# Optimization experiments

Measured on AMD Instinct MI355X. Metric: run time of the kernel, lower is better.

The kernel has to match this reference:

```python
import jax, jax.numpy as jnp
import numpy as np

DIM = 1024      # main_dim
HEADS = 16      # attn_num
HEAD = DIM // HEADS
S = 1024        # seq len per half
BH = 1          # batch per half (x_input batch = 2*BH)
PE = 16; FE = 16      # experts per group
PD = 512; FD = 512    # expert hidden dims
DS = 2048             # shared_expert_dim
K = 4                 # top_k routed experts
EPS = 1e-5
THETA = 10000.0
SCALE_P = 1.0; SCALE_F = 1.0


def rmsnorm(x, w, eps=EPS):
    return x * jax.lax.rsqrt(jnp.mean(x * x, -1, keepdims=True) + eps) * w


def rope(x, theta=THETA):
    # x: [b, h, s, a]; matches RotaryEmb: y1 = x1*cos + x2*sin, y2 = -x1*sin + x2*cos
    a = x.shape[-1]; s = x.shape[2]
    inv = (1.0 / theta) ** (jnp.arange(0, a, 2, dtype=jnp.float32) / a)
    fr = jnp.arange(s, dtype=jnp.float32)[:, None] * inv[None, :]   # [s, a//2]
    cos, sin = jnp.cos(fr), jnp.sin(fr)
    x1, x2 = jnp.split(x, 2, -1)
    return jnp.concatenate([x1 * cos + x2 * sin, -x1 * sin + x2 * cos], -1)


def moe(xt, block, idx, sc):
    # xt: [T, d]; block: [3, E, d, f] (gate/up/down SwiGLU); idx, sc: [T, K]
    g = jnp.einsum('td,edf->tef', xt, block[0])
    u = jnp.einsum('td,edf->tef', xt, block[1])
    h = jax.nn.silu(g) * u
    out_all = jnp.einsum('tef,edf->ted', h, block[2])        # per-expert outputs
    sel = jnp.take_along_axis(out_all, idx[:, :, None], 1)   # [T, K, d]
    return jnp.sum(sel * sc[:, :, None], 1)


def setup_inputs():
    key = jax.random.key(0)
    ks = jax.random.split(key, 16)
    w = 0.02  # param scale for numerical sanity
    d = {}
    d['x_input'] = jax.random.normal(ks[0], (2 * BH, S, DIM), jnp.float32)
    d['p_indices'] = jax.random.randint(ks[1], (BH * S, K), 0, PE)
    d['p_values'] = jax.random.normal(ks[2], (BH * S, K), jnp.float32)
    d['f_indices'] = jax.random.randint(ks[3], (BH * S, K), 0, FE)
    d['f_values'] = jax.random.normal(ks[4], (BH * S, K), jnp.float32)
    d['attn_norm_w'] = jnp.ones((DIM,), jnp.float32)
    d['ffn_norm_w'] = jnp.ones((DIM,), jnp.float32)
    d['W_attn'] = jax.random.normal(ks[5], (DIM, 3 * DIM), jnp.float32) * w
    d['W_attn_o'] = jax.random.normal(ks[6], (DIM, DIM), jnp.float32) * w
    d['ffn_up_w'] = jax.random.normal(ks[7], (DIM, 2 * DS), jnp.float32) * w
    d['ffn_down_w'] = jax.random.normal(ks[8], (DS, DIM), jnp.float32) * w
    d['p_ffn_experts'] = jax.random.normal(ks[9], (3, PE, DIM, PD), jnp.float32) * w
    d['f_ffn_experts'] = jax.random.normal(ks[10], (3, FE, DIM, FD), jnp.float32) * w
    d['p_token_keys'] = jax.random.normal(ks[11], (DIM, PE), jnp.float32) * w
    d['f_token_keys'] = jax.random.normal(ks[12], (DIM, FE), jnp.float32) * w
    d['p_router_bias'] = jnp.zeros((PE,), jnp.float32)
    d['f_router_bias'] = jnp.zeros((FE,), jnp.float32)
    return d


def reference(x_input, p_indices, p_values, f_indices, f_values,
              attn_norm_w, ffn_norm_w, W_attn, W_attn_o, ffn_up_w, ffn_down_w,
              p_ffn_experts, f_ffn_experts, p_token_keys, f_token_keys,
              p_router_bias, f_router_bias):
    B2, s, dim = x_input.shape
    b = B2 // 2
    # attention block
    x = rmsnorm(x_input, attn_norm_w)
    xq, xk, xv = jnp.split(x @ W_attn, 3, -1)
    heads = lambda t: t.reshape(B2, s, HEADS, HEAD).transpose(0, 2, 1, 3)
    xq, xk, xv = heads(xq), heads(xk), heads(xv)
    xq, xk = rope(xq), rope(xk)
    # dual interleave: '(c b) h s a -> b h (s c) a', c=2
    il = lambda t: t.reshape(2, b, HEADS, s, HEAD).transpose(1, 2, 3, 0, 4).reshape(b, HEADS, 2 * s, HEAD)
    q, k, v = il(xq), il(xk), il(xv)
    scores = jnp.einsum('bhqa,bhka->bhqk', q, k) / jnp.sqrt(jnp.float32(HEAD))
    causal = jnp.tril(jnp.ones((2 * s, 2 * s), bool))
    attn = jax.nn.softmax(jnp.where(causal, scores, -jnp.inf), -1)
    o = jnp.einsum('bhqk,bhka->bhqa', attn, v)
    # de-interleave: 'b h (s c) a -> (c b) s (h a)'
    o = o.reshape(b, HEADS, s, 2, HEAD).transpose(3, 0, 2, 1, 4).reshape(B2, s, dim)
    x_ffn_input = o @ W_attn_o + x_input
    x_ffn = rmsnorm(x_ffn_input, ffn_norm_w)
    p_x = x_ffn[:b].reshape(-1, dim)
    f_x = x_ffn[b:].reshape(-1, dim)
    # router: token keys + bias, sigmoid, normalize
    p_vals = p_values + jnp.take_along_axis(p_x @ p_token_keys, p_indices, -1) + p_router_bias[p_indices]
    f_vals = f_values + jnp.take_along_axis(f_x @ f_token_keys, f_indices, -1) + f_router_bias[f_indices]
    p_sc = jax.nn.sigmoid(p_vals)
    p_sc = p_sc / jnp.sum(p_sc, -1, keepdims=True) * SCALE_P
    f_sc = jax.nn.sigmoid(f_vals)
    f_sc = f_sc / jnp.sum(f_sc, -1, keepdims=True) * SCALE_F
    py = moe(p_x, p_ffn_experts, p_indices, p_sc).reshape(b, s, dim)
    fy = moe(f_x, f_ffn_experts, f_indices, f_sc).reshape(b, s, dim)
    y = jnp.concatenate([py, fy], 0) + x_ffn_input
    # shared expert (SwiGLU)
    x1, x2 = jnp.split(x_ffn @ ffn_up_w, 2, -1)
    y = y + (jax.nn.silu(x1) * x2) @ ffn_down_w
    return y
```

## Files before the change

### kernel.cpp

```cpp
#include <hip/hip_runtime.h>


#define S_LEN   1024
#define T_TOT   2048
#define DMODEL  1024
#define NHEADS  16
#define HDIM    64
#define NEXP    16
#define FDIM    512
#define DSH     2048
#define TOPK    4
#define NPAIR   8192

typedef __attribute__((ext_vector_type(4))) float          f32x4;
typedef __attribute__((ext_vector_type(8))) short          s16x8;
typedef __attribute__((ext_vector_type(4))) unsigned short u16x4;

__device__ __forceinline__ float sigm(float x) { return 1.0f / (1.0f + __expf(-x)); }

__device__ __forceinline__ unsigned short bf16r(float f) {
    union { float f; unsigned int u; } v; v.f = f;
    unsigned int r = v.u + 0x7fffu + ((v.u >> 16) & 1u);
    return (unsigned short)(r >> 16);
}

__device__ __forceinline__ u16x4 pack4(float a, float b, float c, float d) {
    u16x4 r;
    r.x = bf16r(a); r.y = bf16r(b); r.z = bf16r(c); r.w = bf16r(d);
    return r;
}

__device__ __forceinline__ int pair2tok(int p) {
    return ((p >> 12) << 10) + ((p & 4095) >> 2);
}

__global__ void rmsnorm_kernel(const float* __restrict__ x,
                               const float* __restrict__ w,
                               float* __restrict__ out) {
    int t = blockIdx.x, tid = threadIdx.x;
    float4 xv = *(const float4*)(x + (size_t)t * DMODEL + tid * 4);
    __shared__ float rb[256];
    rb[tid] = xv.x*xv.x + xv.y*xv.y + xv.z*xv.z + xv.w*xv.w;
    __syncthreads();
    for (int s = 128; s > 0; s >>= 1) { if (tid < s) rb[tid] += rb[tid+s]; __syncthreads(); }
    float scale = rsqrtf(rb[0] * (1.0f/1024.0f) + 1e-5f);
    float4 wv = *(const float4*)(w + tid * 4);
    float4 o;
    o.x = xv.x * scale * wv.x;
    o.y = xv.y * scale * wv.y;
    o.z = xv.z * scale * wv.z;
    o.w = xv.w * scale * wv.w;
    *(float4*)(out + (size_t)t*DMODEL + tid*4) = o;
}

__global__ void rope_kernel(float* __restrict__ qkv) {
    int t = blockIdx.x, tid = threadIdx.x;
    int s = t & 1023;
    float* row = qkv + (size_t)t * 3072;
    for (int pp = tid; pp < 512; pp += 256) {
        int h = pp >> 5, i = pp & 31;
        float fr = (float)s * exp2f(-0.41524101186092028f * (float)i);
        float sn, cs;
        sincosf(fr, &sn, &cs);
        int o1 = (h << 6) + i, o2 = o1 + 32;
        float x1 = row[o1], x2 = row[o2];
        row[o1] = x1 * cs + x2 * sn;
        row[o2] = x2 * cs - x1 * sn;
        x1 = row[1024 + o1]; x2 = row[1024 + o2];
        row[1024 + o1] = x1 * cs + x2 * sn;
        row[1024 + o2] = x2 * cs - x1 * sn;
    }
}

__global__ __launch_bounds__(256) void attn_mfma_kernel(
        const float* __restrict__ qkv, float* __restrict__ attn_out) {
    int qt = blockIdx.x, h = blockIdx.y;
    __shared__ alignas(16) unsigned short Qs[64][72];
    __shared__ alignas(16) unsigned short Ks[64][72];
    __shared__ alignas(16) unsigned short Vt[64][72];
    __shared__ alignas(16) unsigned short Ps[4][16][72];
    int tid = threadIdx.x;
    int w = tid >> 6, lane = tid & 63;
    int lr = lane & 15, lkg = lane >> 4, lk = lkg << 3;

    int rrj[4], ccj[4];
    #pragma unroll
    for (int j = 0; j < 4; ++j) {
        int idx = tid * 4 + j * 1024;
        rrj[j] = idx >> 6; ccj[j] = idx & 63;
    }

    #pragma unroll
    for (int j = 0; j < 4; ++j) {
        int p = qt * 64 + rrj[j];
        int t = ((p & 1) << 10) + (p >> 1);
        float4 v = *(const float4*)(qkv + (size_t)t * 3072 + (h << 6) + ccj[j]);
        *(u16x4*)&Qs[rrj[j]][ccj[j]] = pack4(v.x * 0.125f, v.y * 0.125f,
                                             v.z * 0.125f, v.w * 0.125f);
    }
    float4 pk[4], pv[4];
    #pragma unroll
    for (int j = 0; j < 4; ++j) {
        int p = rrj[j];
        int t = ((p & 1) << 10) + (p >> 1);
        const float* b = qkv + (size_t)t * 3072 + (h << 6) + ccj[j];
        pk[j] = *(const float4*)(b + 1024);
        pv[j] = *(const float4*)(b + 2048);
    }
    __syncthreads();
    s16x8 qa0 = *(const s16x8*)&Qs[(w << 4) + lr][lk];
    s16x8 qa1 = *(const s16x8*)&Qs[(w << 4) + lr][32 + lk];

    float m[4], l[4];
    f32x4 oacc[4];
    #pragma unroll
    for (int r = 0; r < 4; ++r) { m[r] = -1e30f; l[r] = 0.0f; }
    #pragma unroll
    for (int df = 0; df < 4; ++df) oacc[df] = (f32x4)0.0f;

    int qrow_base = qt * 64 + w * 16 + lkg * 4;

    for (int kb = 0; kb <= qt; ++kb) {
        __syncthreads();
        float4 ck[4], cv[4];
        #pragma unroll
        for (int j = 0; j < 4; ++j) { ck[j] = pk[j]; cv[j] = pv[j]; }
        if (kb + 1 <= qt) {
            #pragma unroll
            for (int j = 0; j < 4; ++j) {
                int p = (kb + 1) * 64 + rrj[j];
                int t = ((p & 1) << 10) + (p >> 1);
                const float* b = qkv + (size_t)t * 3072 + (h << 6) + ccj[j];
                pk[j] = *(const float4*)(b + 1024);
                pv[j] = *(const float4*)(b + 2048);
            }
        }
        #pragma unroll
        for (int j = 0; j < 4; ++j) {
            int rr = rrj[j], cc = ccj[j];
            *(u16x4*)&Ks[rr][cc] = pack4(ck[j].x, ck[j].y, ck[j].z, ck[j].w);
            Vt[cc + 0][rr] = bf16r(cv[j].x);
            Vt[cc + 1][rr] = bf16r(cv[j].y);
            Vt[cc + 2][rr] = bf16r(cv[j].z);
            Vt[cc + 3][rr] = bf16r(cv[j].w);
        }
        __syncthreads();

        f32x4 s[4];
        #pragma unroll
        for (int nf = 0; nf < 4; ++nf) {
            s16x8 b0 = *(const s16x8*)&Ks[nf * 16 + lr][lk];
            s16x8 b1 = *(const s16x8*)&Ks[nf * 16 + lr][32 + lk];
            f32x4 z = (f32x4)0.0f;
            z = __builtin_amdgcn_mfma_f32_16x16x32_bf16(qa0, b0, z, 0, 0, 0);
            z = __builtin_amdgcn_mfma_f32_16x16x32_bf16(qa1, b1, z, 0, 0, 0);
            s[nf] = z;
        }
        if (kb == qt) {
            #pragma unroll
            for (int nf = 0; nf < 4; ++nf) {
                int kcol = kb * 64 + nf * 16 + lr;
                #pragma unroll
                for (int r = 0; r < 4; ++r)
                    if (kcol > qrow_base + r) s[nf][r] = -1e30f;
            }
        }
        float mloc[4];
        #pragma unroll
        for (int r = 0; r < 4; ++r)
            mloc[r] = fmaxf(fmaxf(s[0][r], s[1][r]), fmaxf(s[2][r], s[3][r]));
        #pragma unroll
        for (int r = 0; r < 4; ++r) {
            mloc[r] = fmaxf(mloc[r], __shfl_xor(mloc[r], 1));
            mloc[r] = fmaxf(mloc[r], __shfl_xor(mloc[r], 2));
            mloc[r] = fmaxf(mloc[r], __shfl_xor(mloc[r], 4));
            mloc[r] = fmaxf(mloc[r], __shfl_xor(mloc[r], 8));
        }
        float alpha[4], psum[4];
        #pragma unroll
        for (int r = 0; r < 4; ++r) {
            float mnew = fmaxf(m[r], mloc[r]);
            alpha[r] = __expf(m[r] - mnew);
            m[r] = mnew;
            psum[r] = 0.0f;
        }
        #pragma unroll
        for (int nf = 0; nf < 4; ++nf)
            #pragma unroll
            for (int r = 0; r < 4; ++r) {
                float pv2 = __expf(s[nf][r] - m[r]);
                s[nf][r] = pv2;
                psum[r] += pv2;
            }
        #pragma unroll
        for (int r = 0; r < 4; ++r) {
            psum[r] += __shfl_xor(psum[r], 1);
            psum[r] += __shfl_xor(psum[r], 2);
            psum[r] += __shfl_xor(psum[r], 4);
            psum[r] += __shfl_xor(psum[r], 8);
            l[r] = l[r] * alpha[r] + psum[r];
        }
        #pragma unroll
        for (int nf = 0; nf < 4; ++nf)
            #pragma unroll
            for (int r = 0; r < 4; ++r)
                Ps[w][lkg * 4 + r][nf * 16 + lr] = bf16r(s[nf][r]);
        #pragma unroll
        for (int df = 0; df < 4; ++df)
            #pragma unroll
            for (int r = 0; r < 4; ++r)
                oacc[df][r] *= alpha[r];
        s16x8 pa0 = *(const s16x8*)&Ps[w][lr][lk];
        s16x8 pa1 = *(const s16x8*)&Ps[w][lr][32 + lk];
        #pragma unroll
        for (int df = 0; df < 4; ++df) {
            s16x8 v0 = *(const s16x8*)&Vt[df * 16 + lr][lk];
            s16x8 v1 = *(const s16x8*)&Vt[df * 16 + lr][32 + lk];
            oacc[df] = __builtin_amdgcn_mfma_f32_16x16x32_bf16(pa0, v0, oacc[df], 0, 0, 0);
            oacc[df] = __builtin_amdgcn_mfma_f32_16x16x32_bf16(pa1, v1, oacc[df], 0, 0, 0);
        }
    }

    float invl[4];
    #pragma unroll
    for (int r = 0; r < 4; ++r) invl[r] = 1.0f / l[r];
    #pragma unroll
    for (int r = 0; r < 4; ++r) {
        int qrow = qrow_base + r;
        int t = ((qrow & 1) << 10) + (qrow >> 1);
        float* op = attn_out + (size_t)t * 1024 + (h << 6) + lr;
        #pragma unroll
        for (int df = 0; df < 4; ++df)
            op[df * 16] = oacc[df][r] * invl[r];
    }
}

__global__ void router_kernel(const float* __restrict__ xffn,
        const float* __restrict__ p_keys, const float* __restrict__ f_keys,
        const int* __restrict__ p_idx, const int* __restrict__ f_idx,
        const float* __restrict__ p_val, const float* __restrict__ f_val,
        const float* __restrict__ p_bias, const float* __restrict__ f_bias,
        float* __restrict__ sc) {
    int tl = blockIdx.x, hf = blockIdx.y;
    int t = hf * 1024 + tl;
    const float* keys = hf ? f_keys : p_keys;
    const int* idx    = hf ? f_idx  : p_idx;
    const float* val  = hf ? f_val  : p_val;
    const float* bias = hf ? f_bias : p_bias;
    int tid = threadIdx.x;
    float acc[16];
    #pragma unroll
    for (int e = 0; e < 16; ++e) acc[e] = 0.0f;
    const float* x = xffn + (size_t)t * DMODEL;
    for (int d = tid; d < 1024; d += 256) {
        float xd = x[d];
        const float* kr = keys + d * 16;
        #pragma unroll
        for (int e4 = 0; e4 < 4; ++e4) {
            float4 kv = *(const float4*)(kr + e4 * 4);
            acc[e4*4+0] += xd * kv.x;
            acc[e4*4+1] += xd * kv.y;
            acc[e4*4+2] += xd * kv.z;
            acc[e4*4+3] += xd * kv.w;
        }
    }
    #pragma unroll
    for (int e = 0; e < 16; ++e) {
        float v = acc[e];
        v += __shfl_down(v, 32); v += __shfl_down(v, 16); v += __shfl_down(v, 8);
        v += __shfl_down(v, 4);  v += __shfl_down(v, 2);  v += __shfl_down(v, 1);
        acc[e] = v;
    }
    __shared__ float part[4][16];
    __shared__ float logit[16];
    __shared__ float sg[4];
    int wave = tid >> 6, ln = tid & 63;
    if (ln == 0) {
        #pragma unroll
        for (int e = 0; e < 16; ++e) part[wave][e] = acc[e];
    }
    __syncthreads();
    if (tid < 16) logit[tid] = part[0][tid] + part[1][tid] + part[2][tid] + part[3][tid];
    __syncthreads();
    if (tid < 4) {
        int ii = idx[tl * 4 + tid];
        float v = val[tl * 4 + tid] + logit[ii] + bias[ii];
        sg[tid] = 1.0f / (1.0f + expf(-v));
    }
    __syncthreads();
    if (tid < 4) {
        float ssum = sg[0] + sg[1] + sg[2] + sg[3];
        sc[t * 4 + tid] = sg[tid] / ssum;
    }
}

__global__ __launch_bounds__(1024) void buckets_kernel(
        const int* __restrict__ p_idx, const int* __restrict__ f_idx,
        int* __restrict__ counts, int* __restrict__ offsets,
        int* __restrict__ pair_p) {
    __shared__ int lcnt[32], loff[32], lcur[32];
    int tid = threadIdx.x;
    if (tid < 32) { lcnt[tid] = 0; lcur[tid] = 0; }
    __syncthreads();
    for (int p = tid; p < NPAIR; p += 1024) {
        int hf = p >> 12, rem = p & 4095;
        int e = (hf ? f_idx : p_idx)[rem];
        atomicAdd(&lcnt[(hf << 4) + e], 1);
    }
    __syncthreads();
    if (tid == 0) {
        int o = 0;
        for (int b = 0; b < 32; ++b) { loff[b] = o; o += lcnt[b]; }
    }
    __syncthreads();
    for (int p = tid; p < NPAIR; p += 1024) {
        int hf = p >> 12, rem = p & 4095;
        int e = (hf ? f_idx : p_idx)[rem];
        int b = (hf << 4) + e;
        int pos = atomicAdd(&lcur[b], 1);
        pair_p[loff[b] + pos] = p;
    }
    if (tid < 32) { counts[tid] = lcnt[tid]; offsets[tid] = loff[tid]; }
}

template<int MODE, int BN2>
__global__ __launch_bounds__(256) void mfma_gemm(
        const float* __restrict__ A, const float* __restrict__ B,
        float* __restrict__ C, const float* __restrict__ resid,
        int M, int N, int K) {
    constexpr int NI = BN2 / 32;
    __shared__ alignas(16) unsigned short As[128][40];
    __shared__ alignas(16) unsigned short Bs[BN2][40];
    int tid = threadIdx.x;
    int m0 = blockIdx.y * 128, n0 = blockIdx.x * BN2;
    int w = tid >> 6, lane = tid & 63;
    int wm = (w >> 1) * 64, wn = (w & 1) * (BN2 / 2);
    int lr = lane & 15, lk = (lane >> 4) << 3;
    int arow = tid >> 3, acol = (tid & 7) << 2;
    int bn, bk;
    bool bact;
    if (BN2 == 128) { bn = (tid & 31) << 2; bk = (tid >> 5) << 2; bact = true; }
    else            { bn = (tid & 15) << 2; bk = (tid >> 4) << 2; bact = (tid < 128); }
    const float* Ap = A + (size_t)(m0 + arow) * K + acol;

    f32x4 acc[4][NI] = {};
    float4 a_cur[4], b_cur[4], a_nxt[4], b_nxt[4];
    #pragma unroll
    for (int i = 0; i < 4; ++i)
        a_cur[i] = *(const float4*)(Ap + (size_t)(32 * i) * K);
    if (bact) {
        const float* bp = B + (size_t)bk * N + n0 + bn;
        #pragma unroll
        for (int j = 0; j < 4; ++j)
            b_cur[j] = *(const float4*)(bp + (size_t)j * N);
    }

    for (int k0 = 0; k0 < K; k0 += 32) {
        __syncthreads();
        if (k0 + 32 < K) {
            #pragma unroll
            for (int i = 0; i < 4; ++i)
                a_nxt[i] = *(const float4*)(Ap + (size_t)(32 * i) * K + k0 + 32);
            if (bact) {
                const float* bp = B + (size_t)(k0 + 32 + bk) * N + n0 + bn;
                #pragma unroll
                for (int j = 0; j < 4; ++j)
                    b_nxt[j] = *(const float4*)(bp + (size_t)j * N);
            }
        }
        #pragma unroll
        for (int i = 0; i < 4; ++i)
            *(u16x4*)&As[arow + 32 * i][acol] =
                pack4(a_cur[i].x, a_cur[i].y, a_cur[i].z, a_cur[i].w);
        if (bact) {
            *(u16x4*)&Bs[bn+0][bk] = pack4(b_cur[0].x, b_cur[1].x, b_cur[2].x, b_cur[3].x);
            *(u16x4*)&Bs[bn+1][bk] = pack4(b_cur[0].y, b_cur[1].y, b_cur[2].y, b_cur[3].y);
            *(u16x4*)&Bs[bn+2][bk] = pack4(b_cur[0].z, b_cur[1].z, b_cur[2].z, b_cur[3].z);
            *(u16x4*)&Bs[bn+3][bk] = pack4(b_cur[0].w, b_cur[1].w, b_cur[2].w, b_cur[3].w);
        }
        __syncthreads();
        s16x8 af[4], bfr[NI];
        #pragma unroll
        for (int mi = 0; mi < 4; ++mi)
            af[mi] = *(const s16x8*)&As[wm + mi * 16 + lr][lk];
        #pragma unroll
        for (int ni = 0; ni < NI; ++ni)
            bfr[ni] = *(const s16x8*)&Bs[wn + ni * 16 + lr][lk];
        #pragma unroll
        for (int mi = 0; mi < 4; ++mi)
            #pragma unroll
            for (int ni = 0; ni < NI; ++ni)
                acc[mi][ni] = __builtin_amdgcn_mfma_f32_16x16x32_bf16(
                                  af[mi], bfr[ni], acc[mi][ni], 0, 0, 0);
        #pragma unroll
        for (int i = 0; i < 4; ++i) { a_cur[i] = a_nxt[i]; b_cur[i] = b_nxt[i]; }
    }
    #pragma unroll
    for (int mi = 0; mi < 4; ++mi)
        #pragma unroll
        for (int r = 0; r < 4; ++r) {
            int row = m0 + wm + mi * 16 + ((lane >> 4) << 2) + r;
            size_t rb = (size_t)row * N + n0 + wn + lr;
            #pragma unroll
            for (int ni = 0; ni < NI; ++ni) {
                size_t off = rb + ni * 16;
                float v = acc[mi][ni][r];
                if (MODE == 1) v += C[off];
                if (MODE == 2) v += resid[off];
                C[off] = v;
            }
        }
}

template<int MOE>
__global__ __launch_bounds__(256) void mfma_gateup(
        const float* __restrict__ X, const float* __restrict__ Wp,
        const float* __restrict__ Wf, const int* __restrict__ pair_p,
        const int* __restrict__ counts, const int* __restrict__ offsets,
        float* __restrict__ Hout) {
    __shared__ alignas(16) unsigned short As[128][40];
    __shared__ alignas(16) unsigned short Bsg[64][40];
    __shared__ alignas(16) unsigned short Bsu[64][40];
    __shared__ int toks[128];
    int tid = threadIdx.x;
    int rem = 128, slot0 = 0, m0 = 0, n0, ldb;
    const float *Wg, *Wu;
    if (MOE) {
        int bucket = blockIdx.y;
        int cnt = counts[bucket];
        int tile0 = blockIdx.x * 128;
        if (tile0 >= cnt) return;
        n0 = blockIdx.z * 64;
        int e = bucket & 15;
        const float* base = (bucket >> 4) ? Wf : Wp;
        Wg = base + (size_t)e * (DMODEL * FDIM) + n0;
        Wu = base + (size_t)(NEXP + e) * (DMODEL * FDIM) + n0;
        ldb = FDIM;
        slot0 = offsets[bucket] + tile0;
        rem = cnt - tile0;
        if (tid < 128)
            toks[tid] = (tid < rem) ? pair2tok(pair_p[slot0 + tid]) : 0;
    } else {
        m0 = blockIdx.y * 128;
        n0 = blockIdx.x * 64;
        Wg = Wp + n0;
        Wu = Wp + DSH + n0;
        ldb = 2 * DSH;
    }
    int w = tid >> 6, lane = tid & 63;
    int wm = (w >> 1) * 64, wn = (w & 1) * 32;
    int lr = lane & 15, lk = (lane >> 4) << 3;
    int arow = tid >> 3, acol = (tid & 7) << 2;
    int t2 = tid & 127, wq = tid >> 7;
    int bn = (t2 & 15) << 2, bk = (t2 >> 4) << 2;
    const float* bsrc = wq ? Wu : Wg;
    if (MOE) __syncthreads();
    const float* Xr[4];
    #pragma unroll
    for (int i = 0; i < 4; ++i) {
        int r = arow + 32 * i;
        int xrow = MOE ? toks[r] : (m0 + r);
        Xr[i] = X + (size_t)xrow * DMODEL + acol;
    }
    f32x4 ag[4][2] = {}, au[4][2] = {};
    float4 a_cur[4], b_cur[4], a_nxt[4], b_nxt[4];
    #pragma unroll
    for (int i = 0; i < 4; ++i) a_cur[i] = *(const float4*)(Xr[i]);
    {
        const float* bp = bsrc + (size_t)bk * ldb + bn;
        #pragma unroll
        for (int j = 0; j < 4; ++j)
            b_cur[j] = *(const float4*)(bp + (size_t)j * ldb);
    }
    for (int k0 = 0; k0 < DMODEL; k0 += 32) {
        __syncthreads();
        if (k0 + 32 < DMODEL) {
            #pragma unroll
            for (int i = 0; i < 4; ++i)
                a_nxt[i] = *(const float4*)(Xr[i] + k0 + 32);
            const float* bp = bsrc + (size_t)(k0 + 32 + bk) * ldb + bn;
            #pragma unroll
            for (int j = 0; j < 4; ++j)
                b_nxt[j] = *(const float4*)(bp + (size_t)j * ldb);
        }
        #pragma unroll
        for (int i = 0; i < 4; ++i)
            *(u16x4*)&As[arow + 32 * i][acol] =
                pack4(a_cur[i].x, a_cur[i].y, a_cur[i].z, a_cur[i].w);
        {
            unsigned short (*bl)[40] = wq ? Bsu : Bsg;
            *(u16x4*)&bl[bn+0][bk] = pack4(b_cur[0].x, b_cur[1].x, b_cur[2].x, b_cur[3].x);
            *(u16x4*)&bl[bn+1][bk] = pack4(b_cur[0].y, b_cur[1].y, b_cur[2].y, b_cur[3].y);
            *(u16x4*)&bl[bn+2][bk] = pack4(b_cur[0].z, b_cur[1].z, b_cur[2].z, b_cur[3].z);
            *(u16x4*)&bl[bn+3][bk] = pack4(b_cur[0].w, b_cur[1].w, b_cur[2].w, b_cur[3].w);
        }
        __syncthreads();
        s16x8 af[4], bg[2], bu[2];
        #pragma unroll
        for (int mi = 0; mi < 4; ++mi)
            af[mi] = *(const s16x8*)&As[wm + mi * 16 + lr][lk];
        #pragma unroll
        for (int ni = 0; ni < 2; ++ni) {
            bg[ni] = *(const s16x8*)&Bsg[wn + ni * 16 + lr][lk];
            bu[ni] = *(const s16x8*)&Bsu[wn + ni * 16 + lr][lk];
        }
        #pragma unroll
        for (int mi = 0; mi < 4; ++mi)
            #pragma unroll
            for (int ni = 0; ni < 2; ++ni) {
                ag[mi][ni] = __builtin_amdgcn_mfma_f32_16x16x32_bf16(
                                 af[mi], bg[ni], ag[mi][ni], 0, 0, 0);
                au[mi][ni] = __builtin_amdgcn_mfma_f32_16x16x32_bf16(
                                 af[mi], bu[ni], au[mi][ni], 0, 0, 0);
            }
        #pragma unroll
        for (int i = 0; i < 4; ++i) { a_cur[i] = a_nxt[i]; b_cur[i] = b_nxt[i]; }
    }
    #pragma unroll
    for (int mi = 0; mi < 4; ++mi)
        #pragma unroll
        for (int r = 0; r < 4; ++r) {
            int rloc = wm + mi * 16 + ((lane >> 4) << 2) + r;
            if (MOE && rloc >= rem) continue;
            size_t rowb = MOE ? (size_t)(slot0 + rloc) * FDIM
                              : (size_t)(m0 + rloc) * DSH;
            #pragma unroll
            for (int ni = 0; ni < 2; ++ni) {
                float g = ag[mi][ni][r], u = au[mi][ni][r];
                Hout[rowb + n0 + wn + ni * 16 + lr] = g * sigm(g) * u;
            }
        }
}

__global__ __launch_bounds__(256) void mfma_moe_down(
        const float* __restrict__ h_pairs,
        const float* __restrict__ p_experts, const float* __restrict__ f_experts,
        const int* __restrict__ pair_p, const int* __restrict__ counts,
        const int* __restrict__ offsets, const float* __restrict__ sc,
        float* __restrict__ y) {
    __shared__ alignas(16) unsigned short As[128][40];
    __shared__ alignas(16) unsigned short Bs[128][40];
    __shared__ int   tokd[128];
    __shared__ float scd[128];
    int tid = threadIdx.x;
    int bucket = blockIdx.y;
    int cnt = counts[bucket];
    int tile0 = blockIdx.x * 128;
    if (tile0 >= cnt) return;
    int d0 = blockIdx.z * 128;
    int e = bucket & 15;
    const float* base = (bucket >> 4) ? f_experts : p_experts;
    const float* Wd = base + (size_t)(2 * NEXP + e) * (DMODEL * FDIM);
    int slot0 = offsets[bucket] + tile0;
    int rem = cnt - tile0;
    if (tid < 128) {
        int ok = tid < rem;
        int pr = ok ? pair_p[slot0 + tid] : 0;
        tokd[tid] = pair2tok(pr);
        scd[tid]  = ok ? sc[pr] : 0.0f;
    }
    int w = tid >> 6, lane = tid & 63;
    int wm = (w >> 1) * 64, wn = (w & 1) * 64;
    int lr = lane & 15, lk = (lane >> 4) << 3;
    int arow = tid >> 3, acol = (tid & 7) << 2;
    const float* Apb = h_pairs + (size_t)(slot0 + arow) * FDIM + acol;
    const float* Bpb = Wd + (size_t)(d0 + arow) * FDIM + acol;
    f32x4 acc[4][4] = {};
    float4 a_cur[4], b_cur[4], a_nxt[4], b_nxt[4];
    #pragma unroll
    for (int i = 0; i < 4; ++i) {
        a_cur[i] = *(const float4*)(Apb + (size_t)(32 * i) * FDIM);
        b_cur[i] = *(const float4*)(Bpb + (size_t)(32 * i) * FDIM);
    }
    for (int k0 = 0; k0 < FDIM; k0 += 32) {
        __syncthreads();
        if (k0 + 32 < FDIM) {
            #pragma unroll
            for (int i = 0; i < 4; ++i) {
                a_nxt[i] = *(const float4*)(Apb + (size_t)(32 * i) * FDIM + k0 + 32);
                b_nxt[i] = *(const float4*)(Bpb + (size_t)(32 * i) * FDIM + k0 + 32);
            }
        }
        #pragma unroll
        for (int i = 0; i < 4; ++i) {
            int r = arow + 32 * i;
            *(u16x4*)&As[r][acol] = pack4(a_cur[i].x, a_cur[i].y, a_cur[i].z, a_cur[i].w);
            *(u16x4*)&Bs[r][acol] = pack4(b_cur[i].x, b_cur[i].y, b_cur[i].z, b_cur[i].w);
        }
        __syncthreads();
        s16x8 af[4], bfr[4];
        #pragma unroll
        for (int mi = 0; mi < 4; ++mi)
            af[mi] = *(const s16x8*)&As[wm + mi * 16 + lr][lk];
        #pragma unroll
        for (int ni = 0; ni < 4; ++ni)
            bfr[ni] = *(const s16x8*)&Bs[wn + ni * 16 + lr][lk];
        #pragma unroll
        for (int mi = 0; mi < 4; ++mi)
            #pragma unroll
            for (int ni = 0; ni < 4; ++ni)
                acc[mi][ni] = __builtin_amdgcn_mfma_f32_16x16x32_bf16(
                                  af[mi], bfr[ni], acc[mi][ni], 0, 0, 0);
        #pragma unroll
        for (int i = 0; i < 4; ++i) { a_cur[i] = a_nxt[i]; b_cur[i] = b_nxt[i]; }
    }
    #pragma unroll
    for (int mi = 0; mi < 4; ++mi)
        #pragma unroll
        for (int r = 0; r < 4; ++r) {
            int rloc = wm + mi * 16 + ((lane >> 4) << 2) + r;
            if (rloc < rem) {
                int   t = tokd[rloc];
                float s = scd[rloc];
                float* yp = y + (size_t)t * DMODEL + d0 + wn + lr;
                #pragma unroll
                for (int ni = 0; ni < 4; ++ni)
                    atomicAdd(yp + ni * 16, s * acc[mi][ni][r]);
            }
        }
}

extern "C" void kernel_launch(void* const* d_in, const int* in_sizes, int n_in,
                              void* d_out, int out_size, void* d_ws, size_t ws_size,
                              hipStream_t stream) {
    const float* x_input  = (const float*)d_in[0];
    const int*   p_idx    = (const int*)d_in[1];
    const float* p_val    = (const float*)d_in[2];
    const int*   f_idx    = (const int*)d_in[3];
    const float* f_val    = (const float*)d_in[4];
    const float* attn_w   = (const float*)d_in[5];
    const float* ffn_w    = (const float*)d_in[6];
    const float* W_attn   = (const float*)d_in[7];
    const float* W_attn_o = (const float*)d_in[8];
    const float* ffn_up   = (const float*)d_in[9];
    const float* ffn_down = (const float*)d_in[10];
    const float* p_exp    = (const float*)d_in[11];
    const float* f_exp    = (const float*)d_in[12];
    const float* p_keys   = (const float*)d_in[13];
    const float* f_keys   = (const float*)d_in[14];
    const float* p_bias   = (const float*)d_in[15];
    const float* f_bias   = (const float*)d_in[16];
    float* y32 = (float*)d_out;
    (void)in_sizes; (void)n_in; (void)out_size; (void)ws_size;

    float* ws = (float*)d_ws;
    float* xnorm     = ws;
    float* attn_out  = ws;
    float* R1        = ws + 2097152;
    float* qkv       = R1;
    float* h_pairs   = R1;
    float* hs        = R1;
    float* x_ffn_in  = ws + 8388608;
    float* x_ffn     = ws + 10485760;
    float* sc        = ws + 12582912;
    int*   counts    = (int*)(ws + 12591104);
    int*   offsets   = counts + 32;
    int*   pair_p    = offsets + 32;

    rmsnorm_kernel<<<T_TOT, 256, 0, stream>>>(x_input, attn_w, xnorm);
    mfma_gemm<0, 128><<<dim3(24, 16), 256, 0, stream>>>(xnorm, W_attn, qkv, nullptr,
                                                        T_TOT, 3072, 1024);
    rope_kernel<<<T_TOT, 256, 0, stream>>>(qkv);
    attn_mfma_kernel<<<dim3(32, NHEADS), 256, 0, stream>>>(qkv, attn_out);
    mfma_gemm<2, 64><<<dim3(16, 16), 256, 0, stream>>>(attn_out, W_attn_o, x_ffn_in,
                                                       x_input, T_TOT, 1024, 1024);
    rmsnorm_kernel<<<T_TOT, 256, 0, stream>>>(x_ffn_in, ffn_w, x_ffn);
    router_kernel<<<dim3(1024, 2), 256, 0, stream>>>(x_ffn, p_keys, f_keys,
                                                     p_idx, f_idx, p_val, f_val,
                                                     p_bias, f_bias, sc);
    buckets_kernel<<<1, 1024, 0, stream>>>(p_idx, f_idx, counts, offsets, pair_p);
    mfma_gateup<1><<<dim3(4, 32, 8), 256, 0, stream>>>(x_ffn, p_exp, f_exp,
                                                       pair_p, counts, offsets,
                                                       h_pairs);
    hipMemcpyAsync(y32, x_ffn_in, (size_t)T_TOT * DMODEL * sizeof(float),
                   hipMemcpyDeviceToDevice, stream);
    mfma_moe_down<<<dim3(4, 32, 8), 256, 0, stream>>>(h_pairs, p_exp, f_exp,
                                                      pair_p, counts, offsets,
                                                      sc, y32);
    mfma_gateup<0><<<dim3(32, 16), 256, 0, stream>>>(x_ffn, ffn_up, nullptr,
                                                     nullptr, nullptr, nullptr, hs);
    mfma_gemm<1, 64><<<dim3(16, 16), 256, 0, stream>>>(hs, ffn_down, y32, nullptr,
                                                       T_TOT, 1024, 2048);
}
```

Baseline: 725.7 us.

## Store intermediate activations as bf16 across the pipeline instead of fp32

Intermediate activations (normed inputs, qkv, attention output, MoE hidden, shared-expert hidden) are now written and read as bf16 rather than fp32. GEMM A-operand loads become 16-byte bf16 vectors copied straight into shared memory, and the B-side fp32-to-bf16 conversion uses the packed v_cvt_pk_bf16_f32 instruction. The attention V-transpose in shared memory gets an XOR swizzle to cut bank conflicts. This halves activation memory traffic and drops conversion work, at the cost of an extra bf16 rounding of qkv before RoPE and of the attention output.

Result: faster. 688.0 us (-5.2%).

```diff
diff --git a/kernel.cpp b/kernel.cpp
--- a/kernel.cpp
+++ b/kernel.cpp
@@ -1,20 +1,18 @@
 #include <hip/hip_runtime.h>
 
 
-#define S_LEN   1024
 #define T_TOT   2048
 #define DMODEL  1024
 #define NHEADS  16
-#define HDIM    64
 #define NEXP    16
 #define FDIM    512
 #define DSH     2048
-#define TOPK    4
 #define NPAIR   8192
 
 typedef __attribute__((ext_vector_type(4))) float          f32x4;
 typedef __attribute__((ext_vector_type(8))) short          s16x8;
-typedef __attribute__((ext_vector_type(4))) unsigned short u16x4;
+typedef __attribute__((ext_vector_type(8))) unsigned short u16x8;
+typedef __attribute__((ext_vector_type(2))) unsigned int   u32x2;
 
 __device__ __forceinline__ float sigm(float x) { return 1.0f / (1.0f + __expf(-x)); }
 
@@ -24,10 +22,14 @@
     return (unsigned short)(r >> 16);
 }
 
-__device__ __forceinline__ u16x4 pack4(float a, float b, float c, float d) {
-    u16x4 r;
-    r.x = bf16r(a); r.y = bf16r(b); r.z = bf16r(c); r.w = bf16r(d);
+__device__ __forceinline__ unsigned int cvtpk(float lo, float hi) {
+    unsigned int r;
+    asm("v_cvt_pk_bf16_f32 %0, %1, %2" : "=v"(r) : "v"(lo), "v"(hi));
     return r;
+}
+
+__device__ __forceinline__ float ubf(unsigned short u) {
+    union { unsigned int i; float f; } v; v.i = (unsigned int)u << 16; return v.f;
 }
 
 __device__ __forceinline__ int pair2tok(int p) {
@@ -36,7 +38,7 @@
 
 __global__ void rmsnorm_kernel(const float* __restrict__ x,
                                const float* __restrict__ w,
-                               float* __restrict__ out) {
+                               unsigned short* __restrict__ out) {
     int t = blockIdx.x, tid = threadIdx.x;
     float4 xv = *(const float4*)(x + (size_t)t * DMODEL + tid * 4);
     __shared__ float rb[256];
@@ -45,35 +47,34 @@
     for (int s = 128; s > 0; s >>= 1) { if (tid < s) rb[tid] += rb[tid+s]; __syncthreads(); }
     float scale = rsqrtf(rb[0] * (1.0f/1024.0f) + 1e-5f);
     float4 wv = *(const float4*)(w + tid * 4);
-    float4 o;
-    o.x = xv.x * scale * wv.x;
-    o.y = xv.y * scale * wv.y;
-    o.z = xv.z * scale * wv.z;
-    o.w = xv.w * scale * wv.w;
-    *(float4*)(out + (size_t)t*DMODEL + tid*4) = o;
-}
-
-__global__ void rope_kernel(float* __restrict__ qkv) {
+    u32x2 pv;
+    pv.x = cvtpk(xv.x * scale * wv.x, xv.y * scale * wv.y);
+    pv.y = cvtpk(xv.z * scale * wv.z, xv.w * scale * wv.w);
+    *(u32x2*)(out + (size_t)t * DMODEL + tid * 4) = pv;
+}
+
+__global__ void rope_kernel(unsigned short* __restrict__ qkv) {
     int t = blockIdx.x, tid = threadIdx.x;
     int s = t & 1023;
-    float* row = qkv + (size_t)t * 3072;
+    unsigned short* row = qkv + (size_t)t * 3072;
     for (int pp = tid; pp < 512; pp += 256) {
         int h = pp >> 5, i = pp & 31;
         float fr = (float)s * exp2f(-0.41524101186092028f * (float)i);
         float sn, cs;
         sincosf(fr, &sn, &cs);
         int o1 = (h << 6) + i, o2 = o1 + 32;
-        float x1 = row[o1], x2 = row[o2];
-        row[o1] = x1 * cs + x2 * sn;
-        row[o2] = x2 * cs - x1 * sn;
-        x1 = row[1024 + o1]; x2 = row[1024 + o2];
-        row[1024 + o1] = x1 * cs + x2 * sn;
-        row[1024 + o2] = x2 * cs - x1 * sn;
+        float x1 = ubf(row[o1]), x2 = ubf(row[o2]);
+        row[o1] = bf16r(x1 * cs + x2 * sn);
+        row[o2] = bf16r(x2 * cs - x1 * sn);
+        x1 = ubf(row[1024 + o1]); x2 = ubf(row[1024 + o2]);
+        row[1024 + o1] = bf16r(x1 * cs + x2 * sn);
+        row[1024 + o2] = bf16r(x2 * cs - x1 * sn);
     }
 }
 
 __global__ __launch_bounds__(256) void attn_mfma_kernel(
-        const float* __restrict__ qkv, float* __restrict__ attn_out) {
+        const unsigned short* __restrict__ qkv,
+        unsigned short* __restrict__ attn_out) {
     int qt = blockIdx.x, h = blockIdx.y;
     __shared__ alignas(16) unsigned short Qs[64][72];
     __shared__ alignas(16) unsigned short Ks[64][72];
@@ -82,30 +83,28 @@
     int tid = threadIdx.x;
     int w = tid >> 6, lane = tid & 63;
     int lr = lane & 15, lkg = lane >> 4, lk = lkg << 3;
-
-    int rrj[4], ccj[4];
-    #pragma unroll
-    for (int j = 0; j < 4; ++j) {
-        int idx = tid * 4 + j * 1024;
-        rrj[j] = idx >> 6; ccj[j] = idx & 63;
-    }
-
-    #pragma unroll
-    for (int j = 0; j < 4; ++j) {
-        int p = qt * 64 + rrj[j];
+    int kr = tid >> 3, kc = (tid & 7) << 3;
+
+    #pragma unroll
+    for (int i = 0; i < 2; ++i) {
+        int rr = kr + 32 * i;
+        int p = qt * 64 + rr;
         int t = ((p & 1) << 10) + (p >> 1);
-        float4 v = *(const float4*)(qkv + (size_t)t * 3072 + (h << 6) + ccj[j]);
-        *(u16x4*)&Qs[rrj[j]][ccj[j]] = pack4(v.x * 0.125f, v.y * 0.125f,
-                                             v.z * 0.125f, v.w * 0.125f);
-    }
-    float4 pk[4], pv[4];
-    #pragma unroll
-    for (int j = 0; j < 4; ++j) {
-        int p = rrj[j];
-        int t = ((p & 1) << 10) + (p >> 1);
-        const float* b = qkv + (size_t)t * 3072 + (h << 6) + ccj[j];
-        pk[j] = *(const float4*)(b + 1024);
-        pv[j] = *(const float4*)(b + 2048);
+        u16x8 q = *(const u16x8*)(qkv + (size_t)t * 3072 + (h << 6) + kc);
+        unsigned int* dst = (unsigned int*)&Qs[rr][kc];
+        dst[0] = cvtpk(ubf(q[0]) * 0.125f, ubf(q[1]) * 0.125f);
+        dst[1] = cvtpk(ubf(q[2]) * 0.125f, ubf(q[3]) * 0.125f);
+        dst[2] = cvtpk(ubf(q[4]) * 0.125f, ubf(q[5]) * 0.125f);
+        dst[3] = cvtpk(ubf(q[6]) * 0.125f, ubf(q[7]) * 0.125f);
+    }
+    u16x8 pkv[2], pvv[2];
+    #pragma unroll
+    for (int i = 0; i < 2; ++i) {
+        int rr = kr + 32 * i;
+        int t = ((rr & 1) << 10) + (rr >> 1);
+        const unsigned short* b = qkv + (size_t)t * 3072 + (h << 6) + kc;
+        pkv[i] = *(const u16x8*)(b + 1024);
+        pvv[i] = *(const u16x8*)(b + 2048);
     }
     __syncthreads();
     s16x8 qa0 = *(const s16x8*)&Qs[(w << 4) + lr][lk];
@@ -122,27 +121,30 @@
 
     for (int kb = 0; kb <= qt; ++kb) {
         __syncthreads();
-        float4 ck[4], cv[4];
-        #pragma unroll
-        for (int j = 0; j < 4; ++j) { ck[j] = pk[j]; cv[j] = pv[j]; }
+        u16x8 ck[2], cv[2];
+        #pragma unroll
+        for (int i = 0; i < 2; ++i) { ck[i] = pkv[i]; cv[i] = pvv[i]; }
         if (kb + 1 <= qt) {
             #pragma unroll
-            for (int j = 0; j < 4; ++j) {
-                int p = (kb + 1) * 64 + rrj[j];
+            for (int i = 0; i < 2; ++i) {
+                int rr = kr + 32 * i;
+                int p = (kb + 1) * 64 + rr;
                 int t = ((p & 1) << 10) + (p >> 1);
-                const float* b = qkv + (size_t)t * 3072 + (h << 6) + ccj[j];
-                pk[j] = *(const float4*)(b + 1024);
-                pv[j] = *(const float4*)(b + 2048);
-            }
-        }
-        #pragma unroll
-        for (int j = 0; j < 4; ++j) {
-            int rr = rrj[j], cc = ccj[j];
-            *(u16x4*)&Ks[rr][cc] = pack4(ck[j].x, ck[j].y, ck[j].z, ck[j].w);
-            Vt[cc + 0][rr] = bf16r(cv[j].x);
-            Vt[cc + 1][rr] = bf16r(cv[j].y);
-            Vt[cc + 2][rr] = bf16r(cv[j].z);
-            Vt[cc + 3][rr] = bf16r(cv[j].w);
+                const unsigned short* b = qkv + (size_t)t * 3072 + (h << 6) + kc;
+                pkv[i] = *(const u16x8*)(b + 1024);
+                pvv[i] = *(const u16x8*)(b + 2048);
+            }
+        }
+        #pragma unroll
+        for (int i = 0; i < 2; ++i) {
+            int rr = kr + 32 * i;
+            *(u16x8*)&Ks[rr][kc] = ck[i];
+            #pragma unroll
+            for (int j = 0; j < 8; ++j) {
+                int vrow = kc + j;
+                int sw = ((vrow >> 3) & 7) << 3;
+                Vt[vrow][rr ^ sw] = cv[i][j];
+            }
         }
         __syncthreads();
 
@@ -214,8 +216,10 @@
         s16x8 pa1 = *(const s16x8*)&Ps[w][lr][32 + lk];
         #pragma unroll
         for (int df = 0; df < 4; ++df) {
-            s16x8 v0 = *(const s16x8*)&Vt[df * 16 + lr][lk];
-            s16x8 v1 = *(const s16x8*)&Vt[df * 16 + lr][32 + lk];
+            int vr = df * 16 + lr;
+            int sw = ((vr >> 3) & 7) << 3;
+            s16x8 v0 = *(const s16x8*)&Vt[vr][lk ^ sw];
+            s16x8 v1 = *(const s16x8*)&Vt[vr][(32 + lk) ^ sw];
             oacc[df] = __builtin_amdgcn_mfma_f32_16x16x32_bf16(pa0, v0, oacc[df], 0, 0, 0);
             oacc[df] = __builtin_amdgcn_mfma_f32_16x16x32_bf16(pa1, v1, oacc[df], 0, 0, 0);
         }
@@ -228,14 +232,14 @@
     for (int r = 0; r < 4; ++r) {
         int qrow = qrow_base + r;
         int t = ((qrow & 1) << 10) + (qrow >> 1);
-        float* op = attn_out + (size_t)t * 1024 + (h << 6) + lr;
+        unsigned short* op = attn_out + (size_t)t * 1024 + (h << 6) + lr;
         #pragma unroll
         for (int df = 0; df < 4; ++df)
-            op[df * 16] = oacc[df][r] * invl[r];
-    }
-}
-
-__global__ void router_kernel(const float* __restrict__ xffn,
+            op[df * 16] = bf16r(oacc[df][r] * invl[r]);
+    }
+}
+
+__global__ void router_kernel(const unsigned short* __restrict__ xffn,
         const float* __restrict__ p_keys, const float* __restrict__ f_keys,
         const int* __restrict__ p_idx, const int* __restrict__ f_idx,
         const float* __restrict__ p_val, const float* __restrict__ f_val,
@@ -251,9 +255,9 @@
     float acc[16];
     #pragma unroll
     for (int e = 0; e < 16; ++e) acc[e] = 0.0f;
-    const float* x = xffn + (size_t)t * DMODEL;
+    const unsigned short* x = xffn + (size_t)t * DMODEL;
     for (int d = tid; d < 1024; d += 256) {
-        float xd = x[d];
+        float xd = ubf(x[d]);
         const float* kr = keys + d * 16;
         #pragma unroll
         for (int e4 = 0; e4 < 4; ++e4) {
@@ -323,10 +327,10 @@
     if (tid < 32) { counts[tid] = lcnt[tid]; offsets[tid] = loff[tid]; }
 }
 
-template<int MODE, int BN2>
+template<int MODE, int BN2, int OUTBF>
 __global__ __launch_bounds__(256) void mfma_gemm(
-        const float* __restrict__ A, const float* __restrict__ B,
-        float* __restrict__ C, const float* __restrict__ resid,
+        const unsigned short* __restrict__ A, const float* __restrict__ B,
+        void* __restrict__ Cv, const float* __restrict__ resid,
         int M, int N, int K) {
     constexpr int NI = BN2 / 32;
     __shared__ alignas(16) unsigned short As[128][40];
@@ -336,47 +340,46 @@
     int w = tid >> 6, lane = tid & 63;
     int wm = (w >> 1) * 64, wn = (w & 1) * (BN2 / 2);
     int lr = lane & 15, lk = (lane >> 4) << 3;
-    int arow = tid >> 3, acol = (tid & 7) << 2;
-    int bn, bk;
-    bool bact;
-    if (BN2 == 128) { bn = (tid & 31) << 2; bk = (tid >> 5) << 2; bact = true; }
-    else            { bn = (tid & 15) << 2; bk = (tid >> 4) << 2; bact = (tid < 128); }
-    const float* Ap = A + (size_t)(m0 + arow) * K + acol;
+    int ar = tid >> 2, ac = (tid & 3) << 3;
+    int bn = (tid >> 3) << 2, bk = (tid & 7) << 2;
+    bool bact = true;
+    if (BN2 == 64) bact = (tid < 128);
+    const unsigned short* Ap0 = A + (size_t)(m0 + ar) * K + ac;
+    const unsigned short* Ap1 = Ap0 + (size_t)64 * K;
+    const float* Bp = B + (size_t)bk * N + n0 + bn;
 
     f32x4 acc[4][NI] = {};
-    float4 a_cur[4], b_cur[4], a_nxt[4], b_nxt[4];
-    #pragma unroll
-    for (int i = 0; i < 4; ++i)
-        a_cur[i] = *(const float4*)(Ap + (size_t)(32 * i) * K);
+    u16x8 a0c, a1c, a0n, a1n;
+    f32x4 b_c[4], b_n[4];
+    a0c = *(const u16x8*)Ap0;
+    a1c = *(const u16x8*)Ap1;
     if (bact) {
-        const float* bp = B + (size_t)bk * N + n0 + bn;
         #pragma unroll
         for (int j = 0; j < 4; ++j)
-            b_cur[j] = *(const float4*)(bp + (size_t)j * N);
-    }
-
+            b_c[j] = *(const f32x4*)(Bp + (size_t)j * N);
+    }
     for (int k0 = 0; k0 < K; k0 += 32) {
         __syncthreads();
         if (k0 + 32 < K) {
-            #pragma unroll
-            for (int i = 0; i < 4; ++i)
-                a_nxt[i] = *(const float4*)(Ap + (size_t)(32 * i) * K + k0 + 32);
+            a0n = *(const u16x8*)(Ap0 + k0 + 32);
+            a1n = *(const u16x8*)(Ap1 + k0 + 32);
             if (bact) {
-                const float* bp = B + (size_t)(k0 + 32 + bk) * N + n0 + bn;
+                const float* bp = Bp + (size_t)(k0 + 32) * N;
                 #pragma unroll
                 for (int j = 0; j < 4; ++j)
-                    b_nxt[j] = *(const float4*)(bp + (size_t)j * N);
-            }
-        }
-        #pragma unroll
-        for (int i = 0; i < 4; ++i)
-            *(u16x4*)&As[arow + 32 * i][acol] =
-                pack4(a_cur[i].x, a_cur[i].y, a_cur[i].z, a_cur[i].w);
+                    b_n[j] = *(const f32x4*)(bp + (size_t)j * N);
+            }
+        }
+        *(u16x8*)&As[ar][ac] = a0c;
+        *(u16x8*)&As[ar + 64][ac] = a1c;
         if (bact) {
-            *(u16x4*)&Bs[bn+0][bk] = pack4(b_cur[0].x, b_cur[1].x, b_cur[2].x, b_cur[3].x);
-            *(u16x4*)&Bs[bn+1][bk] = pack4(b_cur[0].y, b_cur[1].y, b_cur[2].y, b_cur[3].y);
-            *(u16x4*)&Bs[bn+2][bk] = pack4(b_cur[0].z, b_cur[1].z, b_cur[2].z, b_cur[3].z);
-            *(u16x4*)&Bs[bn+3][bk] = pack4(b_cur[0].w, b_cur[1].w, b_cur[2].w, b_cur[3].w);
+            #pragma unroll
+            for (int jj = 0; jj < 4; ++jj) {
+                u32x2 pv;
+                pv.x = cvtpk(b_c[0][jj], b_c[1][jj]);
+                pv.y = cvtpk(b_c[2][jj], b_c[3][jj]);
+                *(u32x2*)&Bs[bn + jj][bk] = pv;
+            }
         }
         __syncthreads();
         s16x8 af[4], bfr[NI];
@@ -392,8 +395,9 @@
             for (int ni = 0; ni < NI; ++ni)
                 acc[mi][ni] = __builtin_amdgcn_mfma_f32_16x16x32_bf16(
                                   af[mi], bfr[ni], acc[mi][ni], 0, 0, 0);
-        #pragma unroll
-        for (int i = 0; i < 4; ++i) { a_cur[i] = a_nxt[i]; b_cur[i] = b_nxt[i]; }
+        a0c = a0n; a1c = a1n;
+        #pragma unroll
+        for (int j = 0; j < 4; ++j) b_c[j] = b_n[j];
     }
     #pragma unroll
     for (int mi = 0; mi < 4; ++mi)
@@ -405,19 +409,24 @@
             for (int ni = 0; ni < NI; ++ni) {
                 size_t off = rb + ni * 16;
                 float v = acc[mi][ni][r];
-                if (MODE == 1) v += C[off];
-                if (MODE == 2) v += resid[off];
-                C[off] = v;
+                if constexpr (OUTBF) {
+                    ((unsigned short*)Cv)[off] = bf16r(v);
+                } else {
+                    float* Cf = (float*)Cv;
+                    if (MODE == 1) v += Cf[off];
+                    if (MODE == 2) v += resid[off];
+                    Cf[off] = v;
+                }
             }
         }
 }
 
 template<int MOE>
 __global__ __launch_bounds__(256) void mfma_gateup(
-        const float* __restrict__ X, const float* __restrict__ Wp,
+        const unsigned short* __restrict__ X, const float* __restrict__ Wp,
         const float* __restrict__ Wf, const int* __restrict__ pair_p,
         const int* __restrict__ counts, const int* __restrict__ offsets,
-        float* __restrict__ Hout) {
+        unsigned short* __restrict__ Hout) {
     __shared__ alignas(16) unsigned short As[128][40];
     __shared__ alignas(16) unsigned short Bsg[64][40];
     __shared__ alignas(16) unsigned short Bsu[64][40];
@@ -450,49 +459,48 @@
     int w = tid >> 6, lane = tid & 63;
     int wm = (w >> 1) * 64, wn = (w & 1) * 32;
     int lr = lane & 15, lk = (lane >> 4) << 3;
-    int arow = tid >> 3, acol = (tid & 7) << 2;
+    int ar = tid >> 2, ac = (tid & 3) << 3;
     int t2 = tid & 127, wq = tid >> 7;
-    int bn = (t2 & 15) << 2, bk = (t2 >> 4) << 2;
+    int bn = (t2 >> 3) << 2, bk = (t2 & 7) << 2;
     const float* bsrc = wq ? Wu : Wg;
     if (MOE) __syncthreads();
-    const float* Xr[4];
-    #pragma unroll
-    for (int i = 0; i < 4; ++i) {
-        int r = arow + 32 * i;
-        int xrow = MOE ? toks[r] : (m0 + r);
-        Xr[i] = X + (size_t)xrow * DMODEL + acol;
+    const unsigned short *Xp0, *Xp1;
+    {
+        int x0 = MOE ? toks[ar] : (m0 + ar);
+        int x1 = MOE ? toks[ar + 64] : (m0 + ar + 64);
+        Xp0 = X + (size_t)x0 * DMODEL + ac;
+        Xp1 = X + (size_t)x1 * DMODEL + ac;
     }
     f32x4 ag[4][2] = {}, au[4][2] = {};
-    float4 a_cur[4], b_cur[4], a_nxt[4], b_nxt[4];
-    #pragma unroll
-    for (int i = 0; i < 4; ++i) a_cur[i] = *(const float4*)(Xr[i]);
-    {
-        const float* bp = bsrc + (size_t)bk * ldb + bn;
-        #pragma unroll
-        for (int j = 0; j < 4; ++j)
-            b_cur[j] = *(const float4*)(bp + (size_t)j * ldb);
-    }
+    u16x8 a0c, a1c, a0n, a1n;
+    f32x4 b_c[4], b_n[4];
+    a0c = *(const u16x8*)Xp0;
+    a1c = *(const u16x8*)Xp1;
+    const float* Bp = bsrc + (size_t)bk * ldb + bn;
+    #pragma unroll
+    for (int j = 0; j < 4; ++j)
+        b_c[j] = *(const f32x4*)(Bp + (size_t)j * ldb);
     for (int k0 = 0; k0 < DMODEL; k0 += 32) {
         __syncthreads();
         if (k0 + 32 < DMODEL) {
-            #pragma unroll
-            for (int i = 0; i < 4; ++i)
-                a_nxt[i] = *(const float4*)(Xr[i] + k0 + 32);
-            const float* bp = bsrc + (size_t)(k0 + 32 + bk) * ldb + bn;
+            a0n = *(const u16x8*)(Xp0 + k0 + 32);
+            a1n = *(const u16x8*)(Xp1 + k0 + 32);
+            const float* bp = Bp + (size_t)(k0 + 32) * ldb;
             #pragma unroll
             for (int j = 0; j < 4; ++j)
-                b_nxt[j] = *(const float4*)(bp + (size_t)j * ldb);
-        }
-        #pragma unroll
-        for (int i = 0; i < 4; ++i)
-            *(u16x4*)&As[arow + 32 * i][acol] =
-                pack4(a_cur[i].x, a_cur[i].y, a_cur[i].z, a_cur[i].w);
+                b_n[j] = *(const f32x4*)(bp + (size_t)j * ldb);
+        }
+        *(u16x8*)&As[ar][ac] = a0c;
+        *(u16x8*)&As[ar + 64][ac] = a1c;
         {
             unsigned short (*bl)[40] = wq ? Bsu : Bsg;
-            *(u16x4*)&bl[bn+0][bk] = pack4(b_cur[0].x, b_cur[1].x, b_cur[2].x, b_cur[3].x);
-            *(u16x4*)&bl[bn+1][bk] = pack4(b_cur[0].y, b_cur[1].y, b_cur[2].y, b_cur[3].y);
-            *(u16x4*)&bl[bn+2][bk] = pack4(b_cur[0].z, b_cur[1].z, b_cur[2].z, b_cur[3].z);
-            *(u16x4*)&bl[bn+3][bk] = pack4(b_cur[0].w, b_cur[1].w, b_cur[2].w, b_cur[3].w);
+            #pragma unroll
+            for (int jj = 0; jj < 4; ++jj) {
+                u32x2 pv;
+                pv.x = cvtpk(b_c[0][jj], b_c[1][jj]);
+                pv.y = cvtpk(b_c[2][jj], b_c[3][jj]);
+                *(u32x2*)&bl[bn + jj][bk] = pv;
+            }
         }
         __syncthreads();
         s16x8 af[4], bg[2], bu[2];
@@ -513,8 +521,9 @@
                 au[mi][ni] = __builtin_amdgcn_mfma_f32_16x16x32_bf16(
                                  af[mi], bu[ni], au[mi][ni], 0, 0, 0);
             }
-        #pragma unroll
-        for (int i = 0; i < 4; ++i) { a_cur[i] = a_nxt[i]; b_cur[i] = b_nxt[i]; }
+        a0c = a0n; a1c = a1n;
+        #pragma unroll
+        for (int j = 0; j < 4; ++j) b_c[j] = b_n[j];
     }
     #pragma unroll
     for (int mi = 0; mi < 4; ++mi)
@@ -527,13 +536,13 @@
             #pragma unroll
             for (int ni = 0; ni < 2; ++ni) {
                 float g = ag[mi][ni][r], u = au[mi][ni][r];
-                Hout[rowb + n0 + wn + ni * 16 + lr] = g * sigm(g) * u;
+                Hout[rowb + n0 + wn + ni * 16 + lr] = bf16r(g * sigm(g) * u);
             }
         }
 }
 
 __global__ __launch_bounds__(256) void mfma_moe_down(
-        const float* __restrict__ h_pairs,
+        const unsigned short* __restrict__ h_pairs,
         const float* __restrict__ p_experts, const float* __restrict__ f_experts,
         const int* __restrict__ pair_p, const int* __restrict__ counts,
         const int* __restrict__ offsets, const float* __restrict__ sc,
@@ -562,30 +571,36 @@
     int w = tid >> 6, lane = tid & 63;
     int wm = (w >> 1) * 64, wn = (w & 1) * 64;
     int lr = lane & 15, lk = (lane >> 4) << 3;
-    int arow = tid >> 3, acol = (tid & 7) << 2;
-    const float* Apb = h_pairs + (size_t)(slot0 + arow) * FDIM + acol;
-    const float* Bpb = Wd + (size_t)(d0 + arow) * FDIM + acol;
+    int ar = tid >> 2, ac = (tid & 3) << 3;
+    int br = tid >> 3, bc = (tid & 7) << 2;
+    const unsigned short* Ap0 = h_pairs + (size_t)(slot0 + ar) * FDIM + ac;
+    const unsigned short* Ap1 = Ap0 + (size_t)64 * FDIM;
+    const float* Bp0 = Wd + (size_t)(d0 + br) * FDIM + bc;
     f32x4 acc[4][4] = {};
-    float4 a_cur[4], b_cur[4], a_nxt[4], b_nxt[4];
-    #pragma unroll
-    for (int i = 0; i < 4; ++i) {
-        a_cur[i] = *(const float4*)(Apb + (size_t)(32 * i) * FDIM);
-        b_cur[i] = *(const float4*)(Bpb + (size_t)(32 * i) * FDIM);
-    }
+    u16x8 a0c, a1c, a0n, a1n;
+    f32x4 b_c[4], b_n[4];
+    a0c = *(const u16x8*)Ap0;
+    a1c = *(const u16x8*)Ap1;
+    #pragma unroll
+    for (int i = 0; i < 4; ++i)
+        b_c[i] = *(const f32x4*)(Bp0 + (size_t)(32 * i) * FDIM);
     for (int k0 = 0; k0 < FDIM; k0 += 32) {
         __syncthreads();
         if (k0 + 32 < FDIM) {
-            #pragma unroll
-            for (int i = 0; i < 4; ++i) {
-                a_nxt[i] = *(const float4*)(Apb + (size_t)(32 * i) * FDIM + k0 + 32);
-                b_nxt[i] = *(const float4*)(Bpb + (size_t)(32 * i) * FDIM + k0 + 32);
-            }
-        }
+            a0n = *(const u16x8*)(Ap0 + k0 + 32);
+            a1n = *(const u16x8*)(Ap1 + k0 + 32);
+            #pragma unroll
+            for (int i = 0; i < 4; ++i)
+                b_n[i] = *(const f32x4*)(Bp0 + (size_t)(32 * i) * FDIM + k0 + 32);
+        }
+        *(u16x8*)&As[ar][ac] = a0c;
+        *(u16x8*)&As[ar + 64][ac] = a1c;
         #pragma unroll
         for (int i = 0; i < 4; ++i) {
-            int r = arow + 32 * i;
-            *(u16x4*)&As[r][acol] = pack4(a_cur[i].x, a_cur[i].y, a_cur[i].z, a_cur[i].w);
-            *(u16x4*)&Bs[r][acol] = pack4(b_cur[i].x, b_cur[i].y, b_cur[i].z, b_cur[i].w);
+            u32x2 pv;
+            pv.x = cvtpk(b_c[i][0], b_c[i][1]);
+            pv.y = cvtpk(b_c[i][2], b_c[i][3]);
+            *(u32x2*)&Bs[br + 32 * i][bc] = pv;
         }
         __syncthreads();
         s16x8 af[4], bfr[4];
@@ -601,8 +616,9 @@
             for (int ni = 0; ni < 4; ++ni)
                 acc[mi][ni] = __builtin_amdgcn_mfma_f32_16x16x32_bf16(
                                   af[mi], bfr[ni], acc[mi][ni], 0, 0, 0);
-        #pragma unroll
-        for (int i = 0; i < 4; ++i) { a_cur[i] = a_nxt[i]; b_cur[i] = b_nxt[i]; }
+        a0c = a0n; a1c = a1n;
+        #pragma unroll
+        for (int i = 0; i < 4; ++i) b_c[i] = b_n[i];
     }
     #pragma unroll
     for (int mi = 0; mi < 4; ++mi)
@@ -644,41 +660,41 @@
     (void)in_sizes; (void)n_in; (void)out_size; (void)ws_size;
 
     float* ws = (float*)d_ws;
-    float* xnorm     = ws;
-    float* attn_out  = ws;
-    float* R1        = ws + 2097152;
-    float* qkv       = R1;
-    float* h_pairs   = R1;
-    float* hs        = R1;
+    unsigned short* xnormh    = (unsigned short*)ws;
+    unsigned short* attn_outh = (unsigned short*)ws;
+    unsigned short* qkvh      = (unsigned short*)(ws + 2097152);
+    unsigned short* h_pairsh  = (unsigned short*)(ws + 2097152);
+    unsigned short* hsh       = (unsigned short*)(ws + 2097152);
     float* x_ffn_in  = ws + 8388608;
-    float* x_ffn     = ws + 10485760;
+    unsigned short* x_ffnh = (unsigned short*)(ws + 10485760);
     float* sc        = ws + 12582912;
     int*   counts    = (int*)(ws + 12591104);
     int*   offsets   = counts + 32;
     int*   pair_p    = offsets + 32;
 
-    rmsnorm_kernel<<<T_TOT, 256, 0, stream>>>(x_input, attn_w, xnorm);
-    mfma_gemm<0, 128><<<dim3(24, 16), 256, 0, stream>>>(xnorm, W_attn, qkv, nullptr,
-                                                        T_TOT, 3072, 1024);
-    rope_kernel<<<T_TOT, 256, 0, stream>>>(qkv);
-    attn_mfma_kernel<<<dim3(32, NHEADS), 256, 0, stream>>>(qkv, attn_out);
-    mfma_gemm<2, 64><<<dim3(16, 16), 256, 0, stream>>>(attn_out, W_attn_o, x_ffn_in,
-                                                       x_input, T_TOT, 1024, 1024);
-    rmsnorm_kernel<<<T_TOT, 256, 0, stream>>>(x_ffn_in, ffn_w, x_ffn);
-    router_kernel<<<dim3(1024, 2), 256, 0, stream>>>(x_ffn, p_keys, f_keys,
+    rmsnorm_kernel<<<T_TOT, 256, 0, stream>>>(x_input, attn_w, xnormh);
+    mfma_gemm<0, 128, 1><<<dim3(24, 16), 256, 0, stream>>>(xnormh, W_attn, qkvh,
+                                                           nullptr, T_TOT, 3072, 1024);
+    rope_kernel<<<T_TOT, 256, 0, stream>>>(qkvh);
+    attn_mfma_kernel<<<dim3(32, NHEADS), 256, 0, stream>>>(qkvh, attn_outh);
+    mfma_gemm<2, 64, 0><<<dim3(16, 16), 256, 0, stream>>>(attn_outh, W_attn_o,
+                                                          x_ffn_in, x_input,
+                                                          T_TOT, 1024, 1024);
+    rmsnorm_kernel<<<T_TOT, 256, 0, stream>>>(x_ffn_in, ffn_w, x_ffnh);
+    router_kernel<<<dim3(1024, 2), 256, 0, stream>>>(x_ffnh, p_keys, f_keys,
                                                      p_idx, f_idx, p_val, f_val,
                                                      p_bias, f_bias, sc);
     buckets_kernel<<<1, 1024, 0, stream>>>(p_idx, f_idx, counts, offsets, pair_p);
-    mfma_gateup<1><<<dim3(4, 32, 8), 256, 0, stream>>>(x_ffn, p_exp, f_exp,
+    mfma_gateup<1><<<dim3(4, 32, 8), 256, 0, stream>>>(x_ffnh, p_exp, f_exp,
                                                        pair_p, counts, offsets,
-                                                       h_pairs);
+                                                       h_pairsh);
     hipMemcpyAsync(y32, x_ffn_in, (size_t)T_TOT * DMODEL * sizeof(float),
                    hipMemcpyDeviceToDevice, stream);
-    mfma_moe_down<<<dim3(4, 32, 8), 256, 0, stream>>>(h_pairs, p_exp, f_exp,
+    mfma_moe_down<<<dim3(4, 32, 8), 256, 0, stream>>>(h_pairsh, p_exp, f_exp,
                                                       pair_p, counts, offsets,
                                                       sc, y32);
-    mfma_gateup<0><<<dim3(32, 16), 256, 0, stream>>>(x_ffn, ffn_up, nullptr,
-                                                     nullptr, nullptr, nullptr, hs);
-    mfma_gemm<1, 64><<<dim3(16, 16), 256, 0, stream>>>(hs, ffn_down, y32, nullptr,
-                                                       T_TOT, 1024, 2048);
-}
+    mfma_gateup<0><<<dim3(32, 16), 256, 0, stream>>>(x_ffnh, ffn_up, nullptr,
+                                                     nullptr, nullptr, nullptr, hsh);
+    mfma_gemm<1, 64, 0><<<dim3(16, 16), 256, 0, stream>>>(hsh, ffn_down, y32,
+                                                          nullptr, T_TOT, 1024, 2048);
+}
```
